# Kernel optimization log

Measured on AMD Instinct MI355X. Metric: run time of the kernel, lower is better.

Reference implementation:

```python
import jax, jax.numpy as jnp
import numpy as np


def _spline(t, x):
    """Natural cubic spline second derivatives. t: (T,), x: (T, N, D)."""
    T = t.shape[0]
    h = jnp.diff(t)  # (T-1,)
    main = jnp.concatenate([jnp.ones((1,), t.dtype), 2.0 * (h[:-1] + h[1:]), jnp.ones((1,), t.dtype)])
    lower = jnp.concatenate([h[:-1], jnp.zeros((1,), t.dtype)])
    upper = jnp.concatenate([jnp.zeros((1,), t.dtype), h[1:]])
    A = jnp.diag(main) + jnp.diag(lower, -1) + jnp.diag(upper, 1)  # (T, T) tridiagonal, natural BCs
    slopes = (x[1:] - x[:-1]) / h[:, None, None]
    rhs = jnp.concatenate([jnp.zeros_like(x[:1]), 6.0 * (slopes[1:] - slopes[:-1]), jnp.zeros_like(x[:1])], 0)
    M = jnp.linalg.solve(A, rhs.reshape(T, -1)).reshape(x.shape)  # (T, N, D)
    return h, M


def setup_inputs() -> dict:
    key = jax.random.key(0)
    ks = jax.random.split(key, 8)
    B, Amax, T, D, E, H = 32, 64, 16, 10, 128, 512
    t = jnp.arange(T, dtype=jnp.float32)
    x = jax.random.normal(ks[0], (B, Amax, T, D), jnp.float32)
    mask = jax.random.randint(ks[1], (B, Amax), 0, 2) > 0

    def lin(k, o, i):
        k1, k2 = jax.random.split(k)
        s = 1.0 / float(np.sqrt(i))  # torch nn.Linear default init
        return (jax.random.uniform(k1, (o, i), jnp.float32, -s, s),
                jax.random.uniform(k2, (o,), jnp.float32, -s, s))

    W_embed, b_embed = lin(ks[2], E, D)
    W0, b0 = lin(ks[3], H, E)
    W1, b1 = lin(ks[4], H, H)
    W2, b2 = lin(ks[5], H, H)
    W3, b3 = lin(ks[6], E * D, H)
    return dict(t=t, x=x, mask=mask, W_embed=W_embed, b_embed=b_embed,
                W0=W0, b0=b0, W1=W1, b1=b1, W2=W2, b2=b2, W3=W3, b3=b3)


def reference(t, x, mask, W_embed, b_embed, W0, b0, W1, b1, W2, b2, W3, b3):
    B, Amax, T, D = x.shape
    E = W_embed.shape[0]
    xs = x.reshape(B * Amax, T, D).transpose(1, 0, 2)  # (T, N, D)
    h, M = _spline(t, xs)

    def dX_dt(s):
        # derivative of the natural cubic spline at scalar time s -> (N, D)
        i = jnp.clip(jnp.searchsorted(t, s, side='right') - 1, 0, T - 2)
        u = s - t[i]
        hi = h[i]
        b = (xs[i + 1] - xs[i]) / hi - hi * (2.0 * M[i] + M[i + 1]) / 6.0
        return b + M[i] * u + (M[i + 1] - M[i]) * (u * u) / (2.0 * hi)

    def f(z):
        # CDEFunc: linear-relu x3, linear, tanh, view (N, E, D)
        y = jax.nn.relu(z @ W0.T + b0)
        y = jax.nn.relu(y @ W1.T + b1)
        y = jax.nn.relu(y @ W2.T + b2)
        y = jnp.tanh(y @ W3.T + b3)
        return y.reshape(z.shape[0], E, D)

    def vf(s, z):
        # VectorField: f(z) @ dX_dt(s)  -> (N, E)
        return jnp.einsum('ned,nd->ne', f(z), dX_dt(s))

    # spline evaluated at the first knot is just the first observation
    z0 = xs[0] @ W_embed.T + b_embed  # (N, E)

    def step(z, ts):
        # torchdiffeq 'rk4' fixed-step solver (3/8-rule, rk4_alt_step_func)
        t0, t1 = ts
        hs = t1 - t0
        k1 = vf(t0, z)
        k2 = vf(t0 + hs / 3.0, z + hs * k1 / 3.0)
        k3 = vf(t0 + 2.0 * hs / 3.0, z + hs * (k2 - k1 / 3.0))
        k4 = vf(t1, z + hs * (k1 - k2 + k3))
        return z + hs * (k1 + 3.0 * (k2 + k3) + k4) / 8.0, None

    zT, _ = jax.lax.scan(step, z0, (t[:-1], t[1:]))
    # masked-out agents get an all-zero embedding (as in the torch scatter)
    return zT.reshape(B, Amax, E) * mask[..., None].astype(zT.dtype)
```

## Files before the change

### kernel.cpp

```cpp
#include <hip/hip_runtime.h>
#include <hip/hip_bf16.h>


typedef __attribute__((ext_vector_type(4))) float f32x4;
typedef __attribute__((ext_vector_type(8))) short s16x8;

#define N_AG  2048
#define D_IN  10
#define NPTS  46
#define RROWS 8

#define OFF_W0P 0
#define OFF_W1P (128 * 512)
#define OFF_W2P (OFF_W1P + 512 * 512)
#define OFF_W3P (OFF_W2P + 512 * 512)
#define OFF_END (OFF_W3P + 512 * 1280)

__device__ __forceinline__ ushort f2bf(float v) {
  __hip_bfloat16 h = __float2bfloat16(v);
  return *reinterpret_cast<ushort*>(&h);
}

__global__ void pack_w(const float* __restrict__ W, ushort* __restrict__ Wp,
                       int O, int K) {
  int idx = blockIdx.x * blockDim.x + threadIdx.x;
  if (idx >= O * K) return;
  int j    = idx & 7;
  int lane = (idx >> 3) & 63;
  int rest = idx >> 9;
  int KS   = K >> 5;
  int ks   = rest % KS;
  int ct   = rest / KS;
  int col  = (ct << 4) + (lane & 15);
  int k    = (ks << 5) + ((lane >> 4) << 3) + j;
  Wp[idx]  = f2bf(W[col * K + k]);
}

__global__ void spline_dx_k(const float* __restrict__ x, float* __restrict__ dX) {
  int idx = blockIdx.x * blockDim.x + threadIdx.x;
  if (idx >= N_AG * D_IN) return;
  int n = idx / D_IN;
  int d = idx - n * D_IN;

  float xv[16];
#pragma unroll
  for (int t = 0; t < 16; ++t) xv[t] = x[n * 160 + t * 10 + d];

  float cp[15], dp[15], M[16];
  {
    float rhs = 6.0f * (xv[2] - 2.0f * xv[1] + xv[0]);
    cp[1] = 0.25f;
    dp[1] = rhs * 0.25f;
#pragma unroll
    for (int i = 2; i <= 14; ++i) {
      rhs = 6.0f * (xv[i + 1] - 2.0f * xv[i] + xv[i - 1]);
      float m = 1.0f / (4.0f - cp[i - 1]);
      cp[i] = m;
      dp[i] = (rhs - dp[i - 1]) * m;
    }
    M[0] = 0.0f; M[15] = 0.0f;
    M[14] = dp[14];
#pragma unroll
    for (int i = 13; i >= 1; --i) M[i] = dp[i] - cp[i] * M[i + 1];
  }

#pragma unroll
  for (int p = 0; p < NPTS; ++p) {
    int i; float u;
    if (p < 45) { i = p / 3; u = (float)(p % 3) * (1.0f / 3.0f); }
    else        { i = 14;    u = 1.0f; }
    float b = (xv[i + 1] - xv[i]) - (2.0f * M[i] + M[i + 1]) * (1.0f / 6.0f);
    dX[p * (N_AG * D_IN) + idx] = b + M[i] * u + (M[i + 1] - M[i]) * (u * u * 0.5f);
  }
}

template <int KS, int NT, bool VF>
__device__ __forceinline__ void fc(const ushort* __restrict__ Ain, int arowb,
                                   const ushort* __restrict__ Wp,
                                   const float* __restrict__ bias_lds,
                                   ushort* __restrict__ Outb, int orowb,
                                   float (*__restrict__ vf)[128],
                                   const float (*__restrict__ dXs)[D_IN],
                                   int w, int lane, int tbase) {
  f32x4 acc[NT];
#pragma unroll
  for (int t = 0; t < NT; ++t) acc[t] = (f32x4){0.f, 0.f, 0.f, 0.f};

  const int row8 = lane & 7;
  const int g    = lane >> 4;
  const char* abase = (const char*)Ain + row8 * arowb;
  const int aswz = row8 << 4;

#pragma unroll 2
  for (int ks = 0; ks < KS; ++ks) {
    s16x8 a = *(const s16x8*)(abase + (((ks << 6) + (g << 4)) ^ aswz));
#pragma unroll
    for (int t = 0; t < NT; ++t) {
      int ct = w + ((tbase + t) << 3);
      s16x8 b = *(const s16x8*)(Wp + (((ct * KS + ks) * 64 + lane) << 3));
      acc[t] = __builtin_amdgcn_mfma_f32_16x16x32_bf16(a, b, acc[t], 0, 0, 0);
    }
  }

#pragma unroll
  for (int t = 0; t < NT; ++t) {
    int ct  = w + ((tbase + t) << 3);
    int col = (ct << 4) + (lane & 15);
    float bb = bias_lds[col];
#pragma unroll
    for (int r = 0; r < 4; ++r) {
      int orow = (g << 2) + r;
      if (orow < RROWS) {
        float v = acc[t][r] + bb;
        if (!VF) {
          v = fmaxf(v, 0.f);
          int byte = (orow * orowb + (col << 1)) ^ (orow << 4);
          *(ushort*)((char*)Outb + byte) = f2bf(v);
        } else {
          v = 1.0f - 2.0f * __builtin_amdgcn_rcpf(__expf(2.0f * v) + 1.0f);
          int e = col / 10, d = col - e * 10;
          atomicAdd(&vf[orow][e], v * dXs[orow][d]);
        }
      }
    }
  }
}

__global__ __launch_bounds__(512, 2) void cde_mfma(
    const float* __restrict__ x, const int* __restrict__ mask,
    const float* __restrict__ We, const float* __restrict__ be,
    const float* __restrict__ b0, const float* __restrict__ b1,
    const float* __restrict__ b2, const float* __restrict__ b3,
    const ushort* __restrict__ Wp, const float* __restrict__ dX,
    float* __restrict__ out) {
  const int tid  = threadIdx.x;
  const int lane = tid & 63;
  const int w    = tid >> 6;
  const int n0   = blockIdx.x * RROWS;

  __shared__ ushort A0[RROWS * 128];
  __shared__ ushort H1[RROWS * 512];
  __shared__ ushort H2[RROWS * 512];
  __shared__ float  BL[2816];
  __shared__ float  vf[RROWS][128];
  __shared__ float  dXs[RROWS][D_IN];

  float zreg[2], k1r[2], k2r[2], k3r[2];

  {
    int i = tid;
    BL[i] = b0[i]; BL[512 + i] = b1[i]; BL[1024 + i] = b2[i];
    BL[1536 + i] = b3[i];
    BL[2048 + i] = b3[512 + i];
    if (tid < 256) BL[2560 + tid] = b3[1024 + tid];
  }

#pragma unroll
  for (int q = 0; q < 2; ++q) {
    int idx = (q << 9) + tid;
    int e = idx & 127, row = idx >> 7;
    float acc = be[e];
    const float* xr = x + (n0 + row) * 160;
#pragma unroll
    for (int d = 0; d < 10; ++d) acc = fmaf(xr[d], We[e * 10 + d], acc);
    zreg[q] = acc;
    int byte = ((row << 8) + (e << 1)) ^ (row << 4);
    *(ushort*)((char*)A0 + byte) = f2bf(acc);
  }
  __syncthreads();

#pragma unroll 1
  for (int s = 0; s < 15; ++s) {
#pragma unroll 1
    for (int st = 0; st < 4; ++st) {
      if (tid < RROWS * D_IN) {
        int p = (st < 3) ? (3 * s + st) : ((s < 14) ? (3 * s + 3) : 45);
        dXs[tid / 10][tid % 10] = dX[p * (N_AG * D_IN) + n0 * 10 + tid];
      }
      fc<4, 4, false>(A0, 256, Wp + OFF_W0P, BL, H1, 1024, vf, dXs, w, lane, 0);
      __syncthreads();
      fc<16, 4, false>(H1, 1024, Wp + OFF_W1P, BL + 512, H2, 1024, vf, dXs, w, lane, 0);
      __syncthreads();
      fc<16, 4, false>(H2, 1024, Wp + OFF_W2P, BL + 1024, H1, 1024, vf, dXs, w, lane, 0);
      ((float*)vf)[tid] = 0.f;
      ((float*)vf)[512 + tid] = 0.f;
      __syncthreads();
      fc<16, 5, true>(H1, 1024, Wp + OFF_W3P, BL + 1536, nullptr, 0, vf, dXs, w, lane, 0);
      fc<16, 5, true>(H1, 1024, Wp + OFF_W3P, BL + 1536, nullptr, 0, vf, dXs, w, lane, 5);
      __syncthreads();

#pragma unroll
      for (int q = 0; q < 2; ++q) {
        int idx = (q << 9) + tid;
        int e = idx & 127, row = idx >> 7;
        float dv = vf[row][e];
        float z = zreg[q], zin;
        if (st == 0)      { k1r[q] = dv; zin = z + dv * (1.f / 3.f); }
        else if (st == 1) { k2r[q] = dv; zin = z + dv - k1r[q] * (1.f / 3.f); }
        else if (st == 2) { k3r[q] = dv; zin = z + k1r[q] - k2r[q] + dv; }
        else {
          z += (k1r[q] + 3.f * (k2r[q] + k3r[q]) + dv) * 0.125f;
          zreg[q] = z; zin = z;
        }
        int byte = ((row << 8) + (e << 1)) ^ (row << 4);
        *(ushort*)((char*)A0 + byte) = f2bf(zin);
      }
      __syncthreads();
    }
  }

#pragma unroll
  for (int q = 0; q < 2; ++q) {
    int idx = (q << 9) + tid;
    int e = idx & 127, row = idx >> 7;
    out[(n0 + row) * 128 + e] = (mask[n0 + row] != 0) ? zreg[q] : 0.f;
  }
}

extern "C" void kernel_launch(void* const* d_in, const int* in_sizes, int n_in,
                              void* d_out, int out_size, void* d_ws, size_t ws_size,
                              hipStream_t stream) {
  const float* x    = (const float*)d_in[1];
  const int*   mask = (const int*)d_in[2];
  const float* We   = (const float*)d_in[3];
  const float* be   = (const float*)d_in[4];
  const float* W0   = (const float*)d_in[5];
  const float* b0   = (const float*)d_in[6];
  const float* W1   = (const float*)d_in[7];
  const float* b1   = (const float*)d_in[8];
  const float* W2   = (const float*)d_in[9];
  const float* b2   = (const float*)d_in[10];
  const float* W3   = (const float*)d_in[11];
  const float* b3   = (const float*)d_in[12];
  float* out = (float*)d_out;

  ushort* wp = (ushort*)d_ws;
  float*  dX = (float*)((char*)d_ws + (size_t)OFF_END * 2);

  pack_w<<<(128 * 512 + 255) / 256, 256, 0, stream>>>(W0, wp + OFF_W0P, 512, 128);
  pack_w<<<(512 * 512 + 255) / 256, 256, 0, stream>>>(W1, wp + OFF_W1P, 512, 512);
  pack_w<<<(512 * 512 + 255) / 256, 256, 0, stream>>>(W2, wp + OFF_W2P, 512, 512);
  pack_w<<<(512 * 1280 + 255) / 256, 256, 0, stream>>>(W3, wp + OFF_W3P, 1280, 512);
  spline_dx_k<<<(N_AG * D_IN + 255) / 256, 256, 0, stream>>>(x, dX);
  cde_mfma<<<256, 512, 0, stream>>>(x, mask, We, be, b0, b1, b2, b3, wp, dX, out);
}
```

Baseline: 2.333 ms.

## Stream MFMA weight tiles through per-wave LDS ring via async global-to-LDS loads

Replaces the direct global loads of packed weight fragments in each FC layer with a 3-deep per-wave LDS ring buffer. The ring is filled by global_load_lds, gated by explicit vmcnt waits, so weight fetches for future k-steps overlap the MFMA work on the current one. The W3 layer is split into 4+4+2 column-tile calls to fit the ring size. This adds 96KB of LDS (which may limit the launch bound of 2 blocks per CU), hand-tuned wait counts, and an extra LDS round-trip per weight fragment.

Result: slower. 6.856 ms (+193.9%).

```diff
diff --git a/kernel.cpp b/kernel.cpp
--- a/kernel.cpp
+++ b/kernel.cpp
@@ -16,9 +16,20 @@
 #define OFF_W3P (OFF_W2P + 512 * 512)
 #define OFF_END (OFF_W3P + 512 * 1280)
 
+#define VMWAIT(N) do { asm volatile("s_waitcnt vmcnt(" #N ")" ::: "memory"); \
+                       __builtin_amdgcn_sched_barrier(0); } while (0)
+#define LGKM0     do { asm volatile("s_waitcnt lgkmcnt(0)" ::: "memory");    \
+                       __builtin_amdgcn_sched_barrier(0); } while (0)
+
 __device__ __forceinline__ ushort f2bf(float v) {
   __hip_bfloat16 h = __float2bfloat16(v);
   return *reinterpret_cast<ushort*>(&h);
+}
+
+__device__ __forceinline__ void gload_lds16(const void* g, void* l) {
+  __builtin_amdgcn_global_load_lds(
+      (const __attribute__((address_space(1))) unsigned int*)g,
+      (__attribute__((address_space(3))) unsigned int*)l, 16, 0, 0);
 }
 
 __global__ void pack_w(const float* __restrict__ W, ushort* __restrict__ Wp,
@@ -75,13 +86,15 @@
 }
 
 template <int KS, int NT, bool VF>
-__device__ __forceinline__ void fc(const ushort* __restrict__ Ain, int arowb,
-                                   const ushort* __restrict__ Wp,
-                                   const float* __restrict__ bias_lds,
-                                   ushort* __restrict__ Outb, int orowb,
-                                   float (*__restrict__ vf)[128],
-                                   const float (*__restrict__ dXs)[D_IN],
-                                   int w, int lane, int tbase) {
+__device__ __forceinline__ void fc_ring(const ushort* __restrict__ Ain, int arowb,
+                                        const ushort* __restrict__ Wp,
+                                        const float* __restrict__ bias_lds,
+                                        ushort* __restrict__ Outb, int orowb,
+                                        float (*__restrict__ vf)[128],
+                                        const float (*__restrict__ dXs)[D_IN],
+                                        ushort* __restrict__ ring,
+                                        int w, int lane, int tbase) {
+  static_assert(KS >= 3 && (NT == 2 || NT == 4), "");
   f32x4 acc[NT];
 #pragma unroll
   for (int t = 0; t < NT; ++t) acc[t] = (f32x4){0.f, 0.f, 0.f, 0.f};
@@ -91,16 +104,37 @@
   const char* abase = (const char*)Ain + row8 * arowb;
   const int aswz = row8 << 4;
 
-#pragma unroll 2
+#define ISSUE(bb)                                                              \
+  {                                                                            \
+    ushort* s_ = ring + ((bb) % 3) * (NT * 512);                               \
+    _Pragma("unroll")                                                          \
+    for (int t = 0; t < NT; ++t) {                                             \
+      int ct_ = w + ((tbase + t) << 3);                                        \
+      gload_lds16(Wp + (((ct_ * KS + (bb)) * 64 + lane) << 3), s_ + t * 512);  \
+    }                                                                          \
+  }
+
+  ISSUE(0) ISSUE(1) ISSUE(2)
+
+#pragma unroll
   for (int ks = 0; ks < KS; ++ks) {
+    const int rem = KS - 1 - ks;
+    if (rem >= 2)      { if constexpr (NT == 4) VMWAIT(8); else VMWAIT(4); }
+    else if (rem == 1) { if constexpr (NT == 4) VMWAIT(4); else VMWAIT(2); }
+    else               VMWAIT(0);
+
+    const ushort* s = ring + (ks % 3) * (NT * 512);
     s16x8 a = *(const s16x8*)(abase + (((ks << 6) + (g << 4)) ^ aswz));
-#pragma unroll
-    for (int t = 0; t < NT; ++t) {
-      int ct = w + ((tbase + t) << 3);
-      s16x8 b = *(const s16x8*)(Wp + (((ct * KS + ks) * 64 + lane) << 3));
-      acc[t] = __builtin_amdgcn_mfma_f32_16x16x32_bf16(a, b, acc[t], 0, 0, 0);
-    }
-  }
+    s16x8 bfr[NT];
+#pragma unroll
+    for (int t = 0; t < NT; ++t) bfr[t] = *(const s16x8*)(s + t * 512 + lane * 8);
+    LGKM0;
+    if (ks + 3 < KS) ISSUE(ks + 3)
+#pragma unroll
+    for (int t = 0; t < NT; ++t)
+      acc[t] = __builtin_amdgcn_mfma_f32_16x16x32_bf16(a, bfr[t], acc[t], 0, 0, 0);
+  }
+#undef ISSUE
 
 #pragma unroll
   for (int t = 0; t < NT; ++t) {
@@ -141,6 +175,7 @@
   __shared__ ushort A0[RROWS * 128];
   __shared__ ushort H1[RROWS * 512];
   __shared__ ushort H2[RROWS * 512];
+  __shared__ ushort RING[8][3 * 4 * 512];
   __shared__ float  BL[2816];
   __shared__ float  vf[RROWS][128];
   __shared__ float  dXs[RROWS][D_IN];
@@ -168,6 +203,8 @@
     *(ushort*)((char*)A0 + byte) = f2bf(acc);
   }
   __syncthreads();
+
+  ushort* ring = &RING[w][0];
 
 #pragma unroll 1
   for (int s = 0; s < 15; ++s) {
@@ -177,16 +214,17 @@
         int p = (st < 3) ? (3 * s + st) : ((s < 14) ? (3 * s + 3) : 45);
         dXs[tid / 10][tid % 10] = dX[p * (N_AG * D_IN) + n0 * 10 + tid];
       }
-      fc<4, 4, false>(A0, 256, Wp + OFF_W0P, BL, H1, 1024, vf, dXs, w, lane, 0);
-      __syncthreads();
-      fc<16, 4, false>(H1, 1024, Wp + OFF_W1P, BL + 512, H2, 1024, vf, dXs, w, lane, 0);
-      __syncthreads();
-      fc<16, 4, false>(H2, 1024, Wp + OFF_W2P, BL + 1024, H1, 1024, vf, dXs, w, lane, 0);
+      fc_ring<4, 4, false>(A0, 256, Wp + OFF_W0P, BL, H1, 1024, vf, dXs, ring, w, lane, 0);
+      __syncthreads();
+      fc_ring<16, 4, false>(H1, 1024, Wp + OFF_W1P, BL + 512, H2, 1024, vf, dXs, ring, w, lane, 0);
+      __syncthreads();
+      fc_ring<16, 4, false>(H2, 1024, Wp + OFF_W2P, BL + 1024, H1, 1024, vf, dXs, ring, w, lane, 0);
       ((float*)vf)[tid] = 0.f;
       ((float*)vf)[512 + tid] = 0.f;
       __syncthreads();
-      fc<16, 5, true>(H1, 1024, Wp + OFF_W3P, BL + 1536, nullptr, 0, vf, dXs, w, lane, 0);
-      fc<16, 5, true>(H1, 1024, Wp + OFF_W3P, BL + 1536, nullptr, 0, vf, dXs, w, lane, 5);
+      fc_ring<16, 4, true>(H1, 1024, Wp + OFF_W3P, BL + 1536, nullptr, 0, vf, dXs, ring, w, lane, 0);
+      fc_ring<16, 4, true>(H1, 1024, Wp + OFF_W3P, BL + 1536, nullptr, 0, vf, dXs, ring, w, lane, 4);
+      fc_ring<16, 2, true>(H1, 1024, Wp + OFF_W3P, BL + 1536, nullptr, 0, vf, dXs, ring, w, lane, 8);
       __syncthreads();
 
 #pragma unroll
```
